# Optimization experiments

Hardware: AMD Instinct MI355X
Metric: run time of the kernel (lower is better)

The kernel has to match this reference:

```python
import jax, jax.numpy as jnp
import numpy as np

INC, ICS = 32, 8      # in_caps, in_caps_size
ONC, OCS = 32, 16     # out_caps, out_caps_size
K, STRIDE, PAD = 3, 1, 0
ITERS = 3


def squash(t, axis=-1):
    sq = jnp.sum(t * t, axis=axis, keepdims=True)
    return (sq / (1.0 + sq)) * t / jnp.sqrt(sq)


def setup_inputs() -> dict:
    key = jax.random.key(0)
    k1, k2 = jax.random.split(key)
    x = jax.random.normal(k1, (4, INC * ICS, 14, 14), dtype=jnp.float32)
    # nn.Parameter(torch.randn(...)); scaled by 1/sqrt(ICS) for numerical sanity
    weight = jax.random.normal(k2, (ONC, INC * K * K, ICS, OCS), dtype=jnp.float32) * (1.0 / np.sqrt(ICS))
    return {"x": x, "weight": weight}


def reference(x, weight):
    B, C, H, W = x.shape
    OH = (H + 2 * PAD - K) // STRIDE + 1
    OW = (W + 2 * PAD - K) // STRIDE + 1
    # Tile2d: extract KxK patches -> (B, C*K*K, OH, OW), channel order (C, kh, kw)
    patches = jax.lax.conv_general_dilated_patches(
        x, (K, K), (STRIDE, STRIDE), padding=((PAD, PAD), (PAD, PAD)))
    # (B, INC, ICS, K*K, OH*OW) -> (B, OH*OW, K*K, INC, ICS) -> (N, KK*INC, ICS)
    tiles = patches.reshape(B, INC, ICS, K * K, OH * OW)
    tiles = tiles.transpose(0, 4, 3, 1, 2).reshape(B * OH * OW, K * K * INC, ICS)

    # priors: (ONC, N, KKI, OCS)  == x[None,:,:,None,:] @ W[:,None]
    priors = jnp.einsum('nki,okic->onkc', tiles, weight)

    # dynamic routing; logits broadcast over OCS in the original (identical math)
    N = B * OH * OW
    KKI = K * K * INC
    logits = jnp.zeros((ONC, N, KKI, 1), dtype=priors.dtype)
    outputs = None
    for i in range(ITERS):
        probs = jax.nn.softmax(logits, axis=2)              # over KKI routes
        outputs = squash(jnp.sum(probs * priors, axis=2, keepdims=True))  # (ONC,N,1,OCS)
        if i != ITERS - 1:
            logits = logits + jnp.sum(priors * outputs, axis=-1, keepdims=True)

    # (ONC, N, OCS) -> (N, ONC, OCS) -> (B, ONC*OCS, OH, OW)
    out = outputs[:, :, 0, :].transpose(1, 0, 2)
    out = out.reshape(B, OH, OW, ONC * OCS).transpose(0, 3, 1, 2)
    return out
```

## Files before the change

### kernel.cpp

```cpp
#include <hip/hip_runtime.h>

static constexpr int OHW = 12, NSP = 144;

__global__ void build_T(const float* __restrict__ x, float4* __restrict__ T4) {
    const int g = blockIdx.x * 256 + threadIdx.x;
    const int n = g / 576;
    const int q = g - n * 576;
    const int r = q << 2;
    const int k = r >> 3;
    const int i0 = r & 7;
    const int ic = k & 31;
    const int kk = k >> 5;
    const int kh = kk / 3, kw = kk - kh * 3;
    const int b = n / NSP;
    const int rm = n - b * NSP;
    const int oh = rm / OHW, ow = rm - oh * OHW;
    const float* xp = x + (size_t)(b * 256 + ic * 8 + i0) * 196
                        + (oh + kh) * 14 + (ow + kw);
    float4 v;
    v.x = xp[0];
    v.y = xp[196];
    v.z = xp[392];
    v.w = xp[588];
    T4[g] = v;
}

__device__ __forceinline__ void fma4(float4& a, float s, const float4& w) {
    a.x = fmaf(s, w.x, a.x);
    a.y = fmaf(s, w.y, a.y);
    a.z = fmaf(s, w.z, a.z);
    a.w = fmaf(s, w.w, a.w);
}

__device__ __forceinline__ void add4(float4& a, const float4& b) {
    a.x += b.x; a.y += b.y; a.z += b.z; a.w += b.w;
}

__device__ __forceinline__ float dot4(const float4& a, const float4& b) {
    return a.x * b.x + a.y * b.y + a.z * b.z + a.w * b.w;
}

template <int CTRL>
__device__ __forceinline__ float dppmov(float v) {
    return __int_as_float(__builtin_amdgcn_update_dpp(
        0, __float_as_int(v), CTRL, 0xF, 0xF, true));
}

__device__ __forceinline__ float cred(float v) {
    v += dppmov<0xB1>(v);
    v += dppmov<0x4E>(v);
    return v;
}

__device__ __forceinline__ float kred(float v) {
    v += dppmov<0x124>(v);
    v += dppmov<0x128>(v);
#if __has_builtin(__builtin_amdgcn_permlane16_swap)
    {
        auto p = __builtin_amdgcn_permlane16_swap(__float_as_int(v),
                                                  __float_as_int(v),
                                                  false, false);
        v = __int_as_float(p[0]) + __int_as_float(p[1]);
    }
#else
    v += __int_as_float(__builtin_amdgcn_ds_swizzle(__float_as_int(v), 0x401F));
#endif
#if __has_builtin(__builtin_amdgcn_permlane32_swap)
    {
        auto q = __builtin_amdgcn_permlane32_swap(__float_as_int(v),
                                                  __float_as_int(v),
                                                  false, false);
        v = __int_as_float(q[0]) + __int_as_float(q[1]);
    }
#else
    v += __shfl_xor(v, 32);
#endif
    return v;
}

__device__ __forceinline__ void kred4(float4& v) {
    v.x = kred(v.x); v.y = kred(v.y); v.z = kred(v.z); v.w = kred(v.w);
}

__device__ __forceinline__ float4 squash_vq(const float4& svU, float S) {
    const float invS = __frcp_rn(S);
    float4 s;
    s.x = svU.x * invS; s.y = svU.y * invS;
    s.z = svU.z * invS; s.w = svU.w * invS;
    float sq = dot4(s, s);
    sq = cred(sq);
    const float scale = __fsqrt_rn(sq) / (1.0f + sq);
    s.x *= scale; s.y *= scale; s.z *= scale; s.w *= scale;
    return s;
}

__device__ __forceinline__ void do_j(const float4* __restrict__ T4,
                                     const float4* __restrict__ W4,
                                     float4* __restrict__ Pl,
                                     int o, int nbase, int k, int cg,
                                     int g_local, int lane) {
    float4 w[8];
    const float4* wp = W4 + (size_t)(o * 288 + k) * 32 + cg;
    #pragma unroll
    for (int i = 0; i < 8; ++i) w[i] = wp[i * 4];
    #pragma unroll
    for (int nn = 0; nn < 4; ++nn) {
        const float4* tp = T4 + (size_t)(nbase + nn) * 576 + k * 2;
        const float4 t0 = tp[0];
        const float4 t1 = tp[1];
        float4 a = make_float4(0.f, 0.f, 0.f, 0.f);
        fma4(a, t0.x, w[0]); fma4(a, t0.y, w[1]);
        fma4(a, t0.z, w[2]); fma4(a, t0.w, w[3]);
        fma4(a, t1.x, w[4]); fma4(a, t1.y, w[5]);
        fma4(a, t1.z, w[6]); fma4(a, t1.w, w[7]);
        Pl[nn * 512 + g_local * 64 + lane] = a;
    }
}

__global__ __launch_bounds__(256, 4)
void caps_main(const float4* __restrict__ T4, const float4* __restrict__ W4,
               float* __restrict__ out) {
    __shared__ float4 Pl[4 * 8 * 64];
    const int tid = threadIdx.x;
    const int o = blockIdx.y;
    const int nbase = blockIdx.x * 4;
    const int cg = tid & 3;
    const int wv = tid >> 6;
    const int lane = tid & 63;
    const int kgp = lane >> 2;

    float4 P[10];

    do_j(T4, W4, Pl, o, nbase, kgp + 16 * wv, cg, wv, lane);
    do_j(T4, W4, Pl, o, nbase, kgp + 16 * (wv + 4), cg, wv + 4, lane);
    __syncthreads();
    #pragma unroll
    for (int jj = 0; jj < 8; ++jj)
        P[jj] = Pl[wv * 512 + jj * 64 + lane];
    __syncthreads();

    if (wv < 2)
        do_j(T4, W4, Pl, o, nbase, kgp + 16 * (8 + wv), cg, wv, lane);
    __syncthreads();
    P[8] = Pl[wv * 512 + lane];
    P[9] = Pl[wv * 512 + 64 + lane];
    __syncthreads();

    do_j(T4, W4, Pl, o, nbase, kgp + 16 * (10 + wv), cg, wv, lane);
    __builtin_amdgcn_sched_barrier(0);
    do_j(T4, W4, Pl, o, nbase, kgp + 16 * (14 + wv), cg, wv + 4, lane);
    __syncthreads();

    const float4* Pw = Pl + wv * 512 + lane;

    float4 sv = make_float4(0.f, 0.f, 0.f, 0.f);
    #pragma unroll
    for (int jj = 0; jj < 10; ++jj) add4(sv, P[jj]);
    #pragma unroll
    for (int g = 0; g < 8; ++g) add4(sv, Pw[g * 64]);
    kred4(sv);
    float4 vq = squash_vq(sv, 288.0f);

    float lj[18];
    float S = 0.f;
    sv = make_float4(0.f, 0.f, 0.f, 0.f);
    #pragma unroll
    for (int jj = 0; jj < 10; ++jj) {
        float d = dot4(P[jj], vq);
        d = cred(d);
        lj[jj] = d;
        const float e = __expf(d);
        S += e;
        fma4(sv, e, P[jj]);
    }
    #pragma unroll
    for (int g = 0; g < 8; ++g) {
        const float4 q = Pw[g * 64];
        float d = dot4(q, vq);
        d = cred(d);
        lj[10 + g] = d;
        const float e = __expf(d);
        S += e;
        fma4(sv, e, q);
    }
    kred4(sv);
    S = kred(S);
    vq = squash_vq(sv, S);

    S = 0.f;
    sv = make_float4(0.f, 0.f, 0.f, 0.f);
    #pragma unroll
    for (int jj = 0; jj < 10; ++jj) {
        float d = dot4(P[jj], vq);
        d = cred(d);
        const float e = __expf(lj[jj] + d);
        S += e;
        fma4(sv, e, P[jj]);
    }
    #pragma unroll
    for (int g = 0; g < 8; ++g) {
        const float4 q = Pw[g * 64];
        float d = dot4(q, vq);
        d = cred(d);
        const float e = __expf(lj[10 + g] + d);
        S += e;
        fma4(sv, e, q);
    }
    kred4(sv);
    S = kred(S);
    vq = squash_vq(sv, S);

    if (kgp == 0) {
        const int n = nbase + wv;
        const int b = n / NSP;
        const int rm = n - b * NSP;
        float* op = out + (size_t)(b * 512 + o * 16 + cg * 4) * NSP + rm;
        op[0 * NSP] = vq.x;
        op[1 * NSP] = vq.y;
        op[2 * NSP] = vq.z;
        op[3 * NSP] = vq.w;
    }
}

extern "C" void kernel_launch(void* const* d_in, const int* in_sizes, int n_in,
                              void* d_out, int out_size, void* d_ws, size_t ws_size,
                              hipStream_t stream) {
    const float* x  = (const float*)d_in[0];
    const float* wt = (const float*)d_in[1];
    float* out = (float*)d_out;
    float4* T4 = (float4*)d_ws;

    build_T<<<dim3(576 * 576 / 256), 256, 0, stream>>>(x, T4);
    caps_main<<<dim3(144, 32), 256, 0, stream>>>(T4, (const float4*)wt, out);
}
```

Measured before the change: 123.1 us.

## Process eight spatial positions per block and keep all priors in registers

The routing block grows to 512 threads covering eight spatial positions, so each loaded weight slice is reused across eight positions instead of four. The prior computation is re-staged through shared memory in three phases so each wave ends up holding all 18 of its prior float4s in registers. This removes the repeated shared-memory reads during the routing iterations. In exchange it needs more registers per thread, uses a 64KB LDS buffer and launches half as many blocks, which may lower occupancy.

```diff
diff --git a/kernel.cpp b/kernel.cpp
--- a/kernel.cpp
+++ b/kernel.cpp
@@ -94,17 +94,17 @@
     return s;
 }
 
-__device__ __forceinline__ void do_j(const float4* __restrict__ T4,
-                                     const float4* __restrict__ W4,
-                                     float4* __restrict__ Pl,
-                                     int o, int nbase, int k, int cg,
-                                     int g_local, int lane) {
+__device__ __forceinline__ void do_j8(const float4* __restrict__ T4,
+                                      const float4* __restrict__ W4,
+                                      float4* __restrict__ Pl,
+                                      int o, int nbase, int k, int cg,
+                                      int g_local, int lane) {
     float4 w[8];
     const float4* wp = W4 + (size_t)(o * 288 + k) * 32 + cg;
     #pragma unroll
     for (int i = 0; i < 8; ++i) w[i] = wp[i * 4];
     #pragma unroll
-    for (int nn = 0; nn < 4; ++nn) {
+    for (int nn = 0; nn < 8; ++nn) {
         const float4* tp = T4 + (size_t)(nbase + nn) * 576 + k * 2;
         const float4 t0 = tp[0];
         const float4 t1 = tp[1];
@@ -117,47 +117,43 @@
     }
 }
 
-__global__ __launch_bounds__(256, 4)
+__global__ __launch_bounds__(512, 4)
 void caps_main(const float4* __restrict__ T4, const float4* __restrict__ W4,
                float* __restrict__ out) {
-    __shared__ float4 Pl[4 * 8 * 64];
+    __shared__ float4 Pl[8 * 8 * 64];
     const int tid = threadIdx.x;
     const int o = blockIdx.y;
-    const int nbase = blockIdx.x * 4;
+    const int nbase = blockIdx.x * 8;
     const int cg = tid & 3;
     const int wv = tid >> 6;
     const int lane = tid & 63;
     const int kgp = lane >> 2;
 
-    float4 P[10];
-
-    do_j(T4, W4, Pl, o, nbase, kgp + 16 * wv, cg, wv, lane);
-    do_j(T4, W4, Pl, o, nbase, kgp + 16 * (wv + 4), cg, wv + 4, lane);
-    __syncthreads();
-    #pragma unroll
-    for (int jj = 0; jj < 8; ++jj)
-        P[jj] = Pl[wv * 512 + jj * 64 + lane];
-    __syncthreads();
+    float4 P[18];
 
     if (wv < 2)
-        do_j(T4, W4, Pl, o, nbase, kgp + 16 * (8 + wv), cg, wv, lane);
-    __syncthreads();
-    P[8] = Pl[wv * 512 + lane];
-    P[9] = Pl[wv * 512 + 64 + lane];
-    __syncthreads();
-
-    do_j(T4, W4, Pl, o, nbase, kgp + 16 * (10 + wv), cg, wv, lane);
-    __builtin_amdgcn_sched_barrier(0);
-    do_j(T4, W4, Pl, o, nbase, kgp + 16 * (14 + wv), cg, wv + 4, lane);
-    __syncthreads();
-
-    const float4* Pw = Pl + wv * 512 + lane;
+        do_j8(T4, W4, Pl, o, nbase, kgp + 16 * wv, cg, wv, lane);
+    __syncthreads();
+    P[0] = Pl[wv * 512 + lane];
+    P[1] = Pl[wv * 512 + 64 + lane];
+    __syncthreads();
+
+    do_j8(T4, W4, Pl, o, nbase, kgp + 16 * (2 + wv), cg, wv, lane);
+    __syncthreads();
+    #pragma unroll
+    for (int j = 0; j < 8; ++j)
+        P[2 + j] = Pl[wv * 512 + j * 64 + lane];
+    __syncthreads();
+
+    do_j8(T4, W4, Pl, o, nbase, kgp + 16 * (10 + wv), cg, wv, lane);
+    __syncthreads();
+    #pragma unroll
+    for (int j = 0; j < 8; ++j)
+        P[10 + j] = Pl[wv * 512 + j * 64 + lane];
 
     float4 sv = make_float4(0.f, 0.f, 0.f, 0.f);
     #pragma unroll
-    for (int jj = 0; jj < 10; ++jj) add4(sv, P[jj]);
-    #pragma unroll
-    for (int g = 0; g < 8; ++g) add4(sv, Pw[g * 64]);
+    for (int jj = 0; jj < 18; ++jj) add4(sv, P[jj]);
     kred4(sv);
     float4 vq = squash_vq(sv, 288.0f);
 
@@ -165,7 +161,7 @@
     float S = 0.f;
     sv = make_float4(0.f, 0.f, 0.f, 0.f);
     #pragma unroll
-    for (int jj = 0; jj < 10; ++jj) {
+    for (int jj = 0; jj < 18; ++jj) {
         float d = dot4(P[jj], vq);
         d = cred(d);
         lj[jj] = d;
@@ -173,16 +169,6 @@
         S += e;
         fma4(sv, e, P[jj]);
     }
-    #pragma unroll
-    for (int g = 0; g < 8; ++g) {
-        const float4 q = Pw[g * 64];
-        float d = dot4(q, vq);
-        d = cred(d);
-        lj[10 + g] = d;
-        const float e = __expf(d);
-        S += e;
-        fma4(sv, e, q);
-    }
     kred4(sv);
     S = kred(S);
     vq = squash_vq(sv, S);
@@ -190,21 +176,12 @@
     S = 0.f;
     sv = make_float4(0.f, 0.f, 0.f, 0.f);
     #pragma unroll
-    for (int jj = 0; jj < 10; ++jj) {
+    for (int jj = 0; jj < 18; ++jj) {
         float d = dot4(P[jj], vq);
         d = cred(d);
         const float e = __expf(lj[jj] + d);
         S += e;
         fma4(sv, e, P[jj]);
-    }
-    #pragma unroll
-    for (int g = 0; g < 8; ++g) {
-        const float4 q = Pw[g * 64];
-        float d = dot4(q, vq);
-        d = cred(d);
-        const float e = __expf(lj[10 + g] + d);
-        S += e;
-        fma4(sv, e, q);
     }
     kred4(sv);
     S = kred(S);
@@ -231,5 +208,5 @@
     float4* T4 = (float4*)d_ws;
 
     build_T<<<dim3(576 * 576 / 256), 256, 0, stream>>>(x, T4);
-    caps_main<<<dim3(144, 32), 256, 0, stream>>>(T4, (const float4*)wt, out);
-}
+    caps_main<<<dim3(72, 32), 512, 0, stream>>>(T4, (const float4*)wt, out);
+}
```

Result: faster. 119.5 us (-2.9%).
